# Kernel tuning notes

Measured on AMD Instinct MI355X. Metric: run time of the kernel, lower is better.

Reference implementation:

```python
import jax, jax.numpy as jnp
import numpy as np

N, D, H = 512, 512, 1024  # n tokens, per-token dim, hidden; input_dim = 2*D


def setup_inputs() -> dict:
    key = jax.random.key(0)
    k1, k2, k3, k4, k5 = jax.random.split(key, 5)
    inp = jax.random.normal(k1, (N, D), dtype=jnp.float32)
    # torch nn.Linear stores weight [out, in]; we store transposed [in, out]
    s1 = 1.0 / np.sqrt(2 * D)
    W1 = jax.random.uniform(k2, (2 * D, H), dtype=jnp.float32, minval=-s1, maxval=s1)
    b1 = jax.random.uniform(k3, (H,), dtype=jnp.float32, minval=-s1, maxval=s1)
    s2 = 1.0 / np.sqrt(H)
    W2 = jax.random.uniform(k4, (H, 1), dtype=jnp.float32, minval=-s2, maxval=s2)
    b2 = jax.random.uniform(k5, (1,), dtype=jnp.float32, minval=-s2, maxval=s2)
    return {"input": inp, "W1": W1, "b1": b1, "W2": W2, "b2": b2}


def reference(input, W1, b1, W2, b2):
    x = jnp.squeeze(input)                       # [n, d]
    d = x.shape[1]
    # cat(x[i], x[j]) @ W1 == x[i] @ W1[:d] + x[j] @ W1[d:]
    hi = x @ W1[:d]                              # [n, h]
    hj = x @ W1[d:]                              # [n, h]
    h = jnp.tanh(hi[:, None, :] + hj[None, :, :] + b1)  # [n, n, h]
    scores = h @ W2 + b2                         # [n, n, 1]
    return scores[..., 0]                        # [n, n]
```

## Files before the change

### kernel.cpp

```cpp
#include <hip/hip_runtime.h>
#include <math.h>

#define NN 512
#define DD 512
#define HH 1024
#define C2LOG2E 2.8853900817779268f

typedef __attribute__((ext_vector_type(8))) short bf16x8;
typedef __attribute__((ext_vector_type(4))) float f32x4;

static __device__ __forceinline__ float rcp_fast(float x) {
    return __builtin_amdgcn_rcpf(x);
}
static __device__ __forceinline__ float exp2_fast(float x) {
    return __builtin_amdgcn_exp2f(x);
}
static __device__ __forceinline__ ushort f2bf(float f) {
    unsigned u = __float_as_uint(f);
    u += 0x7FFF + ((u >> 16) & 1);
    return (ushort)(u >> 16);
}
static __device__ __forceinline__ float bf2f(short u) {
    return __uint_as_float(((unsigned)(ushort)u) << 16);
}

__global__ __launch_bounds__(256) void k_convert(const float* __restrict__ x,
                                                 const float* __restrict__ W1,
                                                 const float* __restrict__ W2,
                                                 const float* __restrict__ b2,
                                                 short* __restrict__ xbs,
                                                 short* __restrict__ Bts,
                                                 float* __restrict__ out) {
    __shared__ float ts[64][65];
    const int t = threadIdx.x;
    const int bx = blockIdx.x;
    if (bx < 128) {
        const int q = bx * 256 + t;
        const int g = q >> 10, ktc = (q >> 6) & 15, l = q & 63;
        const int i = g * 16 + (l & 15);
        const int k0 = ktc * 32 + (l >> 4) * 8;
        const float4 v0 = *(const float4*)&x[i * DD + k0];
        const float4 v1 = *(const float4*)&x[i * DD + k0 + 4];
        bf16x8 o;
        o[0] = (short)f2bf(v0.x); o[1] = (short)f2bf(v0.y);
        o[2] = (short)f2bf(v0.z); o[3] = (short)f2bf(v0.w);
        o[4] = (short)f2bf(v1.x); o[5] = (short)f2bf(v1.y);
        o[6] = (short)f2bf(v1.z); o[7] = (short)f2bf(v1.w);
        *(bf16x8*)&xbs[q * 8] = o;
        return;
    }
    if (bx >= 384) {
        float* red = &ts[0][0];
        float s = W2[t] + W2[t + 256] + W2[t + 512] + W2[t + 768];
        red[t] = s;
        __syncthreads();
        for (int o = 128; o > 0; o >>= 1) {
            if (t < o) red[t] += red[t + o];
            __syncthreads();
        }
        const float v = b2[0] + red[0];
        const int f4 = (bx - 384) * 256 + t;
        float4 o4; o4.x = v; o4.y = v; o4.z = v; o4.w = v;
        ((float4*)out)[f4] = o4;
        return;
    }
    const int tid = bx - 128;
    const int k0 = (tid >> 5) * 64;
    const int nglob = (tid & 31) * 64;
    const int off = (nglob >= 1024) ? 512 : 0;
    const int nm = nglob & 1023;
#pragma unroll
    for (int u = 0; u < 4; ++u) {
        const int f4 = t + u * 256;
        const int r = f4 >> 4, c = (f4 & 15) * 4;
        *(float4*)&ts[r][c] = *(const float4*)&W1[(off + k0 + r) * HH + nm + c];
    }
    __syncthreads();
#pragma unroll
    for (int u = 0; u < 2; ++u) {
        const int q = u * 256 + t;
        const int lg = q >> 7, lc = (q >> 6) & 1, l = q & 63;
        const int n_loc = lg * 16 + (l & 15);
        const int k_loc = lc * 32 + (l >> 4) * 8;
        bf16x8 o;
#pragma unroll
        for (int j = 0; j < 8; ++j) o[j] = (short)f2bf(ts[k_loc + j][n_loc]);
        const int gg = (nglob >> 4) + lg;
        const int ktc = (k0 >> 5) + lc;
        *(bf16x8*)&Bts[((gg * 16 + ktc) * 64 + l) * 8] = o;
    }
}

__global__ __launch_bounds__(256) void k_gemm_mfma(const short* __restrict__ xbs,
                                                   const short* __restrict__ Bts,
                                                   const float* __restrict__ b1,
                                                   const float* __restrict__ W2,
                                                   short* __restrict__ Ebf) {
    const int t = threadIdx.x;
    const int w = t >> 6, l = t & 63;
    const int gi = blockIdx.x * 4 + w;
    const int by = blockIdx.y;
    const int gn0 = by * 2;

    f32x4 acc[2] = {};
    const short* ap  = xbs + gi * 8192 + l * 8;
    const short* bp0 = Bts + (gn0 + 0) * 8192 + l * 8;
    const short* bp1 = Bts + (gn0 + 1) * 8192 + l * 8;
#pragma unroll
    for (int ktc = 0; ktc < 16; ++ktc) {
        const bf16x8 a = *(const bf16x8*)(ap + ktc * 512);
        acc[0] = __builtin_amdgcn_mfma_f32_16x16x32_bf16(a, *(const bf16x8*)(bp0 + ktc * 512), acc[0], 0, 0, 0);
        acc[1] = __builtin_amdgcn_mfma_f32_16x16x32_bf16(a, *(const bf16x8*)(bp1 + ktc * 512), acc[1], 0, 0, 0);
    }
    const int lm = l & 15;
    const int orow = gi * 16 + (l >> 4) * 4;
    const bool second = (by >= 32);
#pragma unroll
    for (int c = 0; c < 2; ++c) {
        const int n = by * 32 + c * 16 + lm;
#pragma unroll
        for (int r = 0; r < 4; ++r) {
            float val;
            if (second) {
                val = exp2_fast(C2LOG2E * (acc[c][r] + b1[n - HH]));
            } else {
                val = exp2_fast(C2LOG2E * acc[c][r] - 8.0f) * rcp_fast(W2[n]);
            }
            Ebf[(orow + r) * (2 * HH) + n] = (short)f2bf(val);
        }
    }
}

__global__ __launch_bounds__(256) void k_score(const short* __restrict__ Ebf,
                                               const float* __restrict__ W2,
                                               float* __restrict__ out) {
    __shared__ short e1s[64][72];
    __shared__ short e2s[64][72];
    __shared__ float qs[64];
    const int t = threadIdx.x;
    const int i0 = blockIdx.x * 64, j0 = blockIdx.y * 64;
    const int hb = blockIdx.z * 64;
    const int tx = t & 15, ty = t >> 4;

#pragma unroll
    for (int u = 0; u < 2; ++u) {
        const int q = u * 256 + t;
        const int r = q >> 3, c8 = (q & 7) * 8;
        *(bf16x8*)&e1s[r][c8] = *(const bf16x8*)&Ebf[(i0 + r) * (2 * HH) + hb + c8];
        *(bf16x8*)&e2s[r][c8] = *(const bf16x8*)&Ebf[(j0 + r) * (2 * HH) + HH + hb + c8];
    }
    if (t < 64) qs[t] = rcp_fast(W2[hb + t]) * 0.00390625f;
    __syncthreads();

    float acc[4][4] = {};
    const int ty4 = ty * 4;
#pragma unroll 2
    for (int s = 0; s < 8; ++s) {
        const int h8 = s * 8;
        float ef[4][8], ff[4][8];
#pragma unroll
        for (int m = 0; m < 4; ++m) {
            const bf16x8 v = *(const bf16x8*)&e1s[ty4 + m][h8];
#pragma unroll
            for (int j = 0; j < 8; ++j) ef[m][j] = bf2f(v[j]);
        }
#pragma unroll
        for (int n = 0; n < 4; ++n) {
            const bf16x8 v = *(const bf16x8*)&e2s[tx + n * 16][h8];
#pragma unroll
            for (int j = 0; j < 8; ++j) ff[n][j] = bf2f(v[j]);
        }
        float qv[8];
        *(float4*)&qv[0] = *(const float4*)&qs[h8];
        *(float4*)&qv[4] = *(const float4*)&qs[h8 + 4];
#pragma unroll
        for (int m = 0; m < 4; ++m) {
#pragma unroll
            for (int n = 0; n < 4; ++n) {
                const float* em = ef[m];
                const float* fn = ff[n];
                const float d0 = __builtin_fmaf(em[0], fn[0], qv[0]);
                const float d1 = __builtin_fmaf(em[1], fn[1], qv[1]);
                const float d2 = __builtin_fmaf(em[2], fn[2], qv[2]);
                const float d3 = __builtin_fmaf(em[3], fn[3], qv[3]);
                const float d4 = __builtin_fmaf(em[4], fn[4], qv[4]);
                const float d5 = __builtin_fmaf(em[5], fn[5], qv[5]);
                const float d6 = __builtin_fmaf(em[6], fn[6], qv[6]);
                const float d7 = __builtin_fmaf(em[7], fn[7], qv[7]);
                const float a01 = d0 + d1, a23 = d2 + d3;
                const float a45 = d4 + d5, a67 = d6 + d7;
                const float d01 = d0 * d1, d23 = d2 * d3;
                const float d45 = d4 * d5, d67 = d6 * d7;
                const float N1 = __builtin_fmaf(d23, a01, d01 * a23);
                const float N2 = __builtin_fmaf(d67, a45, d45 * a67);
                const float D1 = d01 * d23, D2 = d45 * d67;
                const float Nn = __builtin_fmaf(N1, D2, N2 * D1);
                const float Dd = D1 * D2;
                acc[m][n] = __builtin_fmaf(Nn, rcp_fast(Dd), acc[m][n]);
            }
        }
    }

#pragma unroll
    for (int m = 0; m < 4; ++m) {
        const int row = i0 + ty4 + m;
#pragma unroll
        for (int n = 0; n < 4; ++n) {
            const int col = j0 + tx + n * 16;
            atomicAdd(&out[row * NN + col], -0.0078125f * acc[m][n]);
        }
    }
}

extern "C" void kernel_launch(void* const* d_in, const int* in_sizes, int n_in,
                              void* d_out, int out_size, void* d_ws, size_t ws_size,
                              hipStream_t stream) {
    const float* x  = (const float*)d_in[0];
    const float* W1 = (const float*)d_in[1];
    const float* b1 = (const float*)d_in[2];
    const float* W2 = (const float*)d_in[3];
    const float* b2 = (const float*)d_in[4];
    float* out = (float*)d_out;

    short* Ebf = (short*)d_ws;
    short* xbs = Ebf + NN * 2 * HH;
    short* Bts = xbs + NN * DD;

    k_convert<<<dim3(640), 256, 0, stream>>>(x, W1, W2, b2, xbs, Bts, out);
    k_gemm_mfma<<<dim3(8, 64), 256, 0, stream>>>(xbs, Bts, b1, W2, Ebf);
    k_score<<<dim3(8, 8, 16), 256, 0, stream>>>(Ebf, W2, out);
}
```

Before: 41.61 us.

## Replace atomic accumulation of score partials with per-slice buffers and a combine kernel

The score kernel now writes each hidden-slice partial result to its own 512x512 buffer instead of doing atomicAdd into the output. A new combine kernel sums the 16 partial buffers, adds the bias-derived base value, and writes the output; the output initialisation is removed from the convert kernel. This avoids atomic contention and the dependency on pre-initialised output, at the cost of 16 MB of extra workspace traffic and an additional kernel launch.

```diff
diff --git a/kernel.cpp b/kernel.cpp
--- a/kernel.cpp
+++ b/kernel.cpp
@@ -26,11 +26,8 @@
 
 __global__ __launch_bounds__(256) void k_convert(const float* __restrict__ x,
                                                  const float* __restrict__ W1,
-                                                 const float* __restrict__ W2,
-                                                 const float* __restrict__ b2,
                                                  short* __restrict__ xbs,
-                                                 short* __restrict__ Bts,
-                                                 float* __restrict__ out) {
+                                                 short* __restrict__ Bts) {
     __shared__ float ts[64][65];
     const int t = threadIdx.x;
     const int bx = blockIdx.x;
@@ -49,21 +46,6 @@
         *(bf16x8*)&xbs[q * 8] = o;
         return;
     }
-    if (bx >= 384) {
-        float* red = &ts[0][0];
-        float s = W2[t] + W2[t + 256] + W2[t + 512] + W2[t + 768];
-        red[t] = s;
-        __syncthreads();
-        for (int o = 128; o > 0; o >>= 1) {
-            if (t < o) red[t] += red[t + o];
-            __syncthreads();
-        }
-        const float v = b2[0] + red[0];
-        const int f4 = (bx - 384) * 256 + t;
-        float4 o4; o4.x = v; o4.y = v; o4.z = v; o4.w = v;
-        ((float4*)out)[f4] = o4;
-        return;
-    }
     const int tid = bx - 128;
     const int k0 = (tid >> 5) * 64;
     const int nglob = (tid & 31) * 64;
@@ -133,7 +115,7 @@
 
 __global__ __launch_bounds__(256) void k_score(const short* __restrict__ Ebf,
                                                const float* __restrict__ W2,
-                                               float* __restrict__ out) {
+                                               float* __restrict__ P) {
     __shared__ short e1s[64][72];
     __shared__ short e2s[64][72];
     __shared__ float qs[64];
@@ -201,15 +183,39 @@
         }
     }
 
+    float* __restrict__ Pz = P + blockIdx.z * NN * NN;
 #pragma unroll
     for (int m = 0; m < 4; ++m) {
         const int row = i0 + ty4 + m;
 #pragma unroll
         for (int n = 0; n < 4; ++n) {
             const int col = j0 + tx + n * 16;
-            atomicAdd(&out[row * NN + col], -0.0078125f * acc[m][n]);
-        }
-    }
+            Pz[row * NN + col] = -0.0078125f * acc[m][n];
+        }
+    }
+}
+
+__global__ __launch_bounds__(256) void k_combine(const float* __restrict__ P,
+                                                 const float* __restrict__ W2,
+                                                 const float* __restrict__ b2,
+                                                 float* __restrict__ out) {
+    __shared__ float red[256];
+    const int t = threadIdx.x;
+    red[t] = W2[t] + W2[t + 256] + W2[t + 512] + W2[t + 768];
+    __syncthreads();
+    for (int o = 128; o > 0; o >>= 1) {
+        if (t < o) red[t] += red[t + o];
+        __syncthreads();
+    }
+    const float base = b2[0] + red[0];
+    const int idx = blockIdx.x * 256 + t;
+    float4 s; s.x = base; s.y = base; s.z = base; s.w = base;
+#pragma unroll
+    for (int z = 0; z < 16; ++z) {
+        const float4 p = ((const float4*)(P + z * NN * NN))[idx];
+        s.x += p.x; s.y += p.y; s.z += p.z; s.w += p.w;
+    }
+    ((float4*)out)[idx] = s;
 }
 
 extern "C" void kernel_launch(void* const* d_in, const int* in_sizes, int n_in,
@@ -225,8 +231,10 @@
     short* Ebf = (short*)d_ws;
     short* xbs = Ebf + NN * 2 * HH;
     short* Bts = xbs + NN * DD;
-
-    k_convert<<<dim3(640), 256, 0, stream>>>(x, W1, W2, b2, xbs, Bts, out);
+    float* P   = (float*)(Bts + 2 * HH * DD);
+
+    k_convert<<<dim3(384), 256, 0, stream>>>(x, W1, xbs, Bts);
     k_gemm_mfma<<<dim3(8, 64), 256, 0, stream>>>(xbs, Bts, b1, W2, Ebf);
-    k_score<<<dim3(8, 8, 16), 256, 0, stream>>>(Ebf, W2, out);
-}
+    k_score<<<dim3(8, 8, 16), 256, 0, stream>>>(Ebf, W2, P);
+    k_combine<<<dim3(256), 256, 0, stream>>>(P, W2, b2, out);
+}
```

After: 45.31 us. 8.9% more time.
